# Kernel optimization log

Hardware: AMD Instinct MI355X
Metric: run time of the kernel (lower is better)

Reference implementation:

```python
import jax, jax.numpy as jnp
import numpy as np

B, H, W, D, K = 64, 32, 32, 512, 64
EPS = 1e-12


def setup_inputs() -> dict:
    key = jax.random.key(0)
    k1, k2, k3 = jax.random.split(key, 3)
    inputs = jax.random.normal(k1, (B, H, W, D), dtype=jnp.float32)
    # 1x1 conv kernel (no bias) -> equivalent to a [D, K] matmul per pixel
    w = jax.random.normal(k2, (D, K), dtype=jnp.float32) * 0.02
    # cluster centers, stored in the original as (1,1,1,D,K); we keep [D, K]
    C = jax.random.normal(k3, (D, K), dtype=jnp.float32) * 0.02
    return {"inputs": inputs, "w": w, "C": C}


def _l2norm(v, axis=-1):
    return v / jnp.sqrt(jnp.sum(v * v, axis=axis, keepdims=True) + EPS)


def reference(inputs, w, C):
    # soft-assignment: 1x1 conv + softmax over clusters
    s = jnp.einsum('bhwd,dk->bhwk', inputs, w)          # [B,H,W,K]
    a = jax.nn.softmax(s, axis=-1)
    b, h, ww, d = inputs.shape
    k = w.shape[1]
    a2 = a.reshape(b, h * ww, k)                         # [B,N,K]
    x2 = inputs.reshape(b, h * ww, d)                    # [B,N,D]
    # VLAD reformulation: sum_n a[n,k]*(x[n,d] + C[d,k])
    #  = (a^T x)[k,d] + (sum_n a[n,k]) * C[d,k]
    # avoids materializing the [B,H,W,D,K] broadcast of the original
    vkd = jnp.einsum('bnk,bnd->bkd', a2, x2)             # [B,K,D]
    vkd = vkd + a2.sum(axis=1)[:, :, None] * C.T[None]   # [B,K,D]
    # intra-normalization over D (matches transpose->normalize in original)
    vkd = _l2norm(vkd, axis=-1)
    # transpose back to [B,D,K], flatten, global L2 normalize
    v = jnp.transpose(vkd, (0, 2, 1)).reshape(b, d * k)
    v = _l2norm(v, axis=-1)
    return v
```

## Files before the change

### kernel.cpp

```cpp
#include <hip/hip_runtime.h>

#define EPS 1e-12f
typedef __attribute__((ext_vector_type(8))) short short8;
typedef __attribute__((ext_vector_type(4))) float f32x4;

#define MFMA(a, b, c) __builtin_amdgcn_mfma_f32_16x16x32_bf16(a, b, c, 0, 0, 0)

__device__ __forceinline__ unsigned rne16(unsigned u) {
  return u + 0x7FFFu + ((u >> 16) & 1u);
}
__device__ __forceinline__ void split2(float f, unsigned short& h,
                                       unsigned short& l) {
  unsigned u = __float_as_uint(f);
  unsigned rh = rne16(u);
  float hf = __uint_as_float(rh & 0xFFFF0000u);
  unsigned rl = rne16(__float_as_uint(f - hf));
  h = (unsigned short)(rh >> 16);
  l = (unsigned short)(rl >> 16);
}
__device__ __forceinline__ void split_pair(float f0, float f1,
                                           unsigned& hp, unsigned& lp) {
  unsigned u0 = __float_as_uint(f0), u1 = __float_as_uint(f1);
  unsigned r0 = rne16(u0), r1 = rne16(u1);
  float h0 = __uint_as_float(r0 & 0xFFFF0000u);
  float h1 = __uint_as_float(r1 & 0xFFFF0000u);
  hp = (r0 >> 16) | (r1 & 0xFFFF0000u);
  unsigned v0 = rne16(__float_as_uint(f0 - h0));
  unsigned v1 = rne16(__float_as_uint(f1 - h1));
  lp = (v0 >> 16) | (v1 & 0xFFFF0000u);
}
__device__ __forceinline__ void split8(float4 a, float4 b, short8& h, short8& l) {
  union { unsigned u[4]; short8 s; } H, L;
  split_pair(a.x, a.y, H.u[0], L.u[0]);
  split_pair(a.z, a.w, H.u[1], L.u[1]);
  split_pair(b.x, b.y, H.u[2], L.u[2]);
  split_pair(b.z, b.w, H.u[3], L.u[3]);
  h = H.s; l = L.s;
}

extern "C" __global__ __launch_bounds__(256) void netvlad_prep(
    const float* __restrict__ w, unsigned short* __restrict__ wTh,
    unsigned short* __restrict__ wTl)
{
  int tg = blockIdx.x * 256 + threadIdx.x;
  int k = tg >> 9, d = tg & 511;
  unsigned short h, l;
  split2(w[d * 64 + k], h, l);
  wTh[tg] = h;
  wTl[tg] = l;
}

extern "C" __global__ __launch_bounds__(256) void netvlad_assign(
    const float* __restrict__ x, const unsigned short* __restrict__ wTh,
    const unsigned short* __restrict__ wTl, unsigned short* __restrict__ aTh,
    unsigned short* __restrict__ aTl, float* __restrict__ asum)
{
  __shared__ unsigned short ath[64 * 72];
  __shared__ unsigned short atl[64 * 72];
  __shared__ float asp[4 * 64];

  const int t = threadIdx.x;
  const int lane = t & 63, wv = t >> 6;
  const int lo4 = lane & 15, hi4 = lane >> 4;
  const int b = blockIdx.x >> 4;
  const int nblk = (blockIdx.x & 15) << 6;

  f32x4 acc[4] = {};

  const float* xp =
      x + ((size_t)(blockIdx.x << 6) + (wv << 4) + lo4) * 512 + (hi4 << 3);

  float4 c0 = *(const float4*)xp;
  float4 c1 = *(const float4*)(xp + 4);
  for (int d0 = 0; d0 < 512; d0 += 32) {
    const float* np = xp + ((d0 < 480) ? d0 + 32 : 0);
    float4 n0v = *(const float4*)np;
    float4 n1v = *(const float4*)(np + 4);
    short8 xh, xl;
    split8(c0, c1, xh, xl);
#pragma unroll
    for (int nt = 0; nt < 4; ++nt) {
      const size_t wo = (size_t)((nt << 4) + lo4) * 512 + d0 + (hi4 << 3);
      short8 wh = *(const short8*)(wTh + wo);
      short8 wl = *(const short8*)(wTl + wo);
      acc[nt] = MFMA(xh, wh, acc[nt]);
      acc[nt] = MFMA(xl, wh, acc[nt]);
      acc[nt] = MFMA(xh, wl, acc[nt]);
    }
    c0 = n0v; c1 = n1v;
  }

  float asum_p[4] = {0.f, 0.f, 0.f, 0.f};
#pragma unroll
  for (int r = 0; r < 4; ++r) {
    float s0 = acc[0][r], s1 = acc[1][r], s2 = acc[2][r], s3 = acc[3][r];
    float m = fmaxf(fmaxf(s0, s1), fmaxf(s2, s3));
    m = fmaxf(m, __shfl_xor(m, 1));
    m = fmaxf(m, __shfl_xor(m, 2));
    m = fmaxf(m, __shfl_xor(m, 4));
    m = fmaxf(m, __shfl_xor(m, 8));
    float e0 = __expf(s0 - m), e1 = __expf(s1 - m);
    float e2 = __expf(s2 - m), e3 = __expf(s3 - m);
    float s = e0 + e1 + e2 + e3;
    s += __shfl_xor(s, 1);
    s += __shfl_xor(s, 2);
    s += __shfl_xor(s, 4);
    s += __shfl_xor(s, 8);
    float inv = 1.0f / s;
    e0 *= inv; e1 *= inv; e2 *= inv; e3 *= inv;
    asum_p[0] += e0; asum_p[1] += e1; asum_p[2] += e2; asum_p[3] += e3;
    acc[0][r] = e0; acc[1][r] = e1; acc[2][r] = e2; acc[3][r] = e3;
  }
#pragma unroll
  for (int nt = 0; nt < 4; ++nt)
#pragma unroll
    for (int r = 0; r < 4; ++r) {
      unsigned short h, l;
      split2(acc[nt][r], h, l);
      int idx = ((nt << 4) + lo4) * 72 + (wv << 4) + (hi4 << 2) + r;
      ath[idx] = h;
      atl[idx] = l;
    }
#pragma unroll
  for (int nt = 0; nt < 4; ++nt) {
    float v = asum_p[nt];
    v += __shfl_xor(v, 16);
    v += __shfl_xor(v, 32);
    if (lane < 16) asp[(wv << 6) + (nt << 4) + lane] = v;
  }
  __syncthreads();
  if (t < 64) {
    float s = asp[t] + asp[64 + t] + asp[128 + t] + asp[192 + t];
    atomicAdd(&asum[(b << 6) + t], s);
  }
  {
    const int k = t >> 2, px0 = (t & 3) << 4;
    const size_t go = ((size_t)((b << 6) + k) << 10) + nblk + px0;
    *(short8*)(aTh + go)     = *(short8*)&ath[k * 72 + px0];
    *(short8*)(aTh + go + 8) = *(short8*)&ath[k * 72 + px0 + 8];
    *(short8*)(aTl + go)     = *(short8*)&atl[k * 72 + px0];
    *(short8*)(aTl + go + 8) = *(short8*)&atl[k * 72 + px0 + 8];
  }
}

extern "C" __global__ __launch_bounds__(256) void netvlad_vlad(
    const float* __restrict__ x, const unsigned short* __restrict__ aTh,
    const unsigned short* __restrict__ aTl, float* __restrict__ vkd)
{
  __shared__ unsigned short xth[2][32 * 72];
  __shared__ unsigned short xtl[2][32 * 72];
  const int t = threadIdx.x;
  const int lane = t & 63, wv = t >> 6;
  const int lo4 = lane & 15, hi4 = lane >> 4;
  const int b = blockIdx.x >> 4;
  const int ds = (blockIdx.x & 15) << 5;
  const int tn = t & 63;
  const int tdc = (t >> 6) << 3;
  const float* xsb = x + ((size_t)(b << 10)) * 512 + ds + tdc;

  f32x4 acc[2] = {};

  float4 r0 = *(const float4*)(xsb + (size_t)tn * 512);
  float4 r1 = *(const float4*)(xsb + (size_t)tn * 512 + 4);

  for (int it = 0; it < 16; ++it) {
    const int n0 = it << 6;
    unsigned short* th = xth[it & 1];
    unsigned short* tl = xtl[it & 1];
    float f[8] = {r0.x, r0.y, r0.z, r0.w, r1.x, r1.y, r1.z, r1.w};
#pragma unroll
    for (int j = 0; j < 8; ++j) {
      unsigned short h, l;
      split2(f[j], h, l);
      th[(tdc + j) * 72 + tn] = h;
      tl[(tdc + j) * 72 + tn] = l;
    }
    __syncthreads();
    if (it < 15) {
      const float* p = xsb + (size_t)(n0 + 64 + tn) * 512;
      r0 = *(const float4*)p;
      r1 = *(const float4*)(p + 4);
    }
#pragma unroll
    for (int nf = 0; nf < 2; ++nf) {
      const size_t ao = ((size_t)((b << 6) + (wv << 4) + lo4) << 10)
                      + n0 + (nf << 5) + (hi4 << 3);
      short8 ah = *(const short8*)(aTh + ao);
      short8 al = *(const short8*)(aTl + ao);
#pragma unroll
      for (int dt = 0; dt < 2; ++dt) {
        const int xo = ((dt << 4) + lo4) * 72 + (nf << 5) + (hi4 << 3);
        short8 bh = *(short8*)&th[xo];
        short8 bl = *(short8*)&tl[xo];
        acc[dt] = MFMA(ah, bh, acc[dt]);
        acc[dt] = MFMA(ah, bl, acc[dt]);
        acc[dt] = MFMA(al, bh, acc[dt]);
      }
    }
  }
#pragma unroll
  for (int dt = 0; dt < 2; ++dt) {
    float* vb = vkd + (((size_t)(b << 9) + ds + (dt << 4) + lo4) << 6)
              + (wv << 4) + (hi4 << 2);
    *(float4*)vb = make_float4(acc[dt][0], acc[dt][1], acc[dt][2], acc[dt][3]);
  }
}

extern "C" __global__ __launch_bounds__(256) void netvlad_fin1(
    const float* __restrict__ vkd, const float* __restrict__ Cm,
    const float* __restrict__ asum, float* __restrict__ out,
    float* __restrict__ r_buf)
{
  __shared__ float rp[16 * 64];
  const int t = threadIdx.x;
  const int b = blockIdx.x >> 4;
  const int ds = (blockIdx.x & 15) << 5;
  const int k4 = (t & 15) << 2;
  const int dg = t >> 4;
  float4 asv = *(const float4*)(asum + (b << 6) + k4);
  float4 racc = {0.f, 0.f, 0.f, 0.f};
#pragma unroll
  for (int j = 0; j < 2; ++j) {
    int d = ds + dg * 2 + j;
    size_t off = (((size_t)(b << 9) + d) << 6) + k4;
    float4 v = *(const float4*)(vkd + off);
    float4 c = *(const float4*)(Cm + ((size_t)d << 6) + k4);
    v.x += asv.x * c.x; v.y += asv.y * c.y;
    v.z += asv.z * c.z; v.w += asv.w * c.w;
    *(float4*)(out + off) = v;
    racc.x = fmaf(v.x, v.x, racc.x); racc.y = fmaf(v.y, v.y, racc.y);
    racc.z = fmaf(v.z, v.z, racc.z); racc.w = fmaf(v.w, v.w, racc.w);
  }
  *(float4*)&rp[dg * 64 + k4] = racc;
  __syncthreads();
  if (t < 64) {
    float r = 0.f;
#pragma unroll
    for (int g = 0; g < 16; ++g) r += rp[g * 64 + t];
    atomicAdd(&r_buf[(b << 6) + t], r);
  }
}

extern "C" __global__ __launch_bounds__(256) void netvlad_fin3(
    float* __restrict__ out, const float* __restrict__ r_buf)
{
  __shared__ float sc[64];
  const int t = threadIdx.x;
  const int b = blockIdx.x >> 3;
  if (t < 64) {
    float r = r_buf[(b << 6) + t];
    float g = r / (r + EPS);
    g += __shfl_xor(g, 1);
    g += __shfl_xor(g, 2);
    g += __shfl_xor(g, 4);
    g += __shfl_xor(g, 8);
    g += __shfl_xor(g, 16);
    g += __shfl_xor(g, 32);
    sc[t] = 1.0f / (sqrtf(r + EPS) * sqrtf(g + EPS));
  }
  __syncthreads();
  float4* o4 = (float4*)out;
#pragma unroll
  for (int c = 0; c < 4; ++c) {
    int idx = blockIdx.x * 1024 + c * 256 + t;
    float4 v = o4[idx];
    int k4 = (idx & 15) * 4;
    v.x *= sc[k4]; v.y *= sc[k4 + 1]; v.z *= sc[k4 + 2]; v.w *= sc[k4 + 3];
    o4[idx] = v;
  }
}

extern "C" void kernel_launch(void* const* d_in, const int* in_sizes, int n_in,
                              void* d_out, int out_size, void* d_ws,
                              size_t ws_size, hipStream_t stream)
{
  const float* x  = (const float*)d_in[0];
  const float* w  = (const float*)d_in[1];
  const float* Cm = (const float*)d_in[2];
  float* out = (float*)d_out;

  unsigned short* aTh = (unsigned short*)d_ws;
  unsigned short* aTl = aTh + 4194304;
  float* vkd = (float*)(aTl + 4194304);
  unsigned short* wTh = (unsigned short*)(vkd + 2097152);
  unsigned short* wTl = wTh + 32768;
  float* asum = (float*)(wTl + 32768);
  float* r_buf = asum + 4096;

  hipMemsetAsync(asum, 0, 2 * 4096 * sizeof(float), stream);

  netvlad_prep  <<< 128, 256, 0, stream>>>(w, wTh, wTl);
  netvlad_assign<<<1024, 256, 0, stream>>>(x, wTh, wTl, aTh, aTl, asum);
  netvlad_vlad  <<<1024, 256, 0, stream>>>(x, aTh, aTl, vkd);
  netvlad_fin1  <<<1024, 256, 0, stream>>>(vkd, Cm, asum, out, r_buf);
  netvlad_fin3  <<< 512, 256, 0, stream>>>(out, r_buf);
}
```

Baseline: 294.6 us.

## Double-buffer weight and assignment fragments in registers across assign and vlad loops

In the assign kernel, the w-fragment loads for the next 32-wide d step are now prefetched into double-buffered registers alongside the x prefetch, and the loop is fully unrolled. In the vlad kernel, the assignment fragments are prefetched one iteration ahead, and the x tile staging into LDS is reorganised so each thread writes packed pixel pairs into rows padded to 74 shorts. Both kernels get a 4-blocks-per-CU occupancy hint. The aim is to hide global-load latency behind the MFMA work. The cost is higher register pressure, and 128-bit LDS reads at a 148-byte row stride are no longer 16-byte aligned.

```diff
diff --git a/kernel.cpp b/kernel.cpp
--- a/kernel.cpp
+++ b/kernel.cpp
@@ -50,7 +50,7 @@
   wTl[tg] = l;
 }
 
-extern "C" __global__ __launch_bounds__(256) void netvlad_assign(
+extern "C" __global__ __launch_bounds__(256, 4) void netvlad_assign(
     const float* __restrict__ x, const unsigned short* __restrict__ wTh,
     const unsigned short* __restrict__ wTl, unsigned short* __restrict__ aTh,
     unsigned short* __restrict__ aTl, float* __restrict__ asum)
@@ -69,25 +69,39 @@
 
   const float* xp =
       x + ((size_t)(blockIdx.x << 6) + (wv << 4) + lo4) * 512 + (hi4 << 3);
-
-  float4 c0 = *(const float4*)xp;
-  float4 c1 = *(const float4*)(xp + 4);
-  for (int d0 = 0; d0 < 512; d0 += 32) {
-    const float* np = xp + ((d0 < 480) ? d0 + 32 : 0);
-    float4 n0v = *(const float4*)np;
-    float4 n1v = *(const float4*)(np + 4);
+  const unsigned short* wph = wTh + (lo4 << 9) + (hi4 << 3);
+  const unsigned short* wpl = wTl + (lo4 << 9) + (hi4 << 3);
+
+  float4 xc0[2], xc1[2];
+  short8 wh[2][4], wl[2][4];
+
+  xc0[0] = *(const float4*)xp;
+  xc1[0] = *(const float4*)(xp + 4);
+#pragma unroll
+  for (int nt = 0; nt < 4; ++nt) {
+    wh[0][nt] = *(const short8*)(wph + nt * 8192);
+    wl[0][nt] = *(const short8*)(wpl + nt * 8192);
+  }
+
+#pragma unroll
+  for (int it = 0; it < 16; ++it) {
+    const int cur = it & 1, nxt = cur ^ 1;
+    const int dn = ((it + 1) & 15) << 5;
+    xc0[nxt] = *(const float4*)(xp + dn);
+    xc1[nxt] = *(const float4*)(xp + dn + 4);
+#pragma unroll
+    for (int nt = 0; nt < 4; ++nt) {
+      wh[nxt][nt] = *(const short8*)(wph + nt * 8192 + dn);
+      wl[nxt][nt] = *(const short8*)(wpl + nt * 8192 + dn);
+    }
     short8 xh, xl;
-    split8(c0, c1, xh, xl);
+    split8(xc0[cur], xc1[cur], xh, xl);
 #pragma unroll
     for (int nt = 0; nt < 4; ++nt) {
-      const size_t wo = (size_t)((nt << 4) + lo4) * 512 + d0 + (hi4 << 3);
-      short8 wh = *(const short8*)(wTh + wo);
-      short8 wl = *(const short8*)(wTl + wo);
-      acc[nt] = MFMA(xh, wh, acc[nt]);
-      acc[nt] = MFMA(xl, wh, acc[nt]);
-      acc[nt] = MFMA(xh, wl, acc[nt]);
-    }
-    c0 = n0v; c1 = n1v;
+      acc[nt] = MFMA(xh, wh[cur][nt], acc[nt]);
+      acc[nt] = MFMA(xl, wh[cur][nt], acc[nt]);
+      acc[nt] = MFMA(xh, wl[cur][nt], acc[nt]);
+    }
   }
 
   float asum_p[4] = {0.f, 0.f, 0.f, 0.f};
@@ -143,60 +157,81 @@
   }
 }
 
-extern "C" __global__ __launch_bounds__(256) void netvlad_vlad(
+extern "C" __global__ __launch_bounds__(256, 4) void netvlad_vlad(
     const float* __restrict__ x, const unsigned short* __restrict__ aTh,
     const unsigned short* __restrict__ aTl, float* __restrict__ vkd)
 {
-  __shared__ unsigned short xth[2][32 * 72];
-  __shared__ unsigned short xtl[2][32 * 72];
+  __shared__ unsigned short xth[2][32 * 74];
+  __shared__ unsigned short xtl[2][32 * 74];
   const int t = threadIdx.x;
   const int lane = t & 63, wv = t >> 6;
   const int lo4 = lane & 15, hi4 = lane >> 4;
   const int b = blockIdx.x >> 4;
   const int ds = (blockIdx.x & 15) << 5;
-  const int tn = t & 63;
-  const int tdc = (t >> 6) << 3;
-  const float* xsb = x + ((size_t)(b << 10)) * 512 + ds + tdc;
+  const int np2 = (t & 31) << 1;
+  const int dc = (t >> 5) << 2;
+  const float* xsb = x + ((size_t)(b << 10)) * 512 + ds + dc;
+  const unsigned short* aph =
+      aTh + ((size_t)((b << 6) + (wv << 4) + lo4) << 10) + (hi4 << 3);
+  const unsigned short* apl =
+      aTl + ((size_t)((b << 6) + (wv << 4) + lo4) << 10) + (hi4 << 3);
 
   f32x4 acc[2] = {};
-
-  float4 r0 = *(const float4*)(xsb + (size_t)tn * 512);
-  float4 r1 = *(const float4*)(xsb + (size_t)tn * 512 + 4);
-
+  float4 xr0, xr1;
+  short8 ah[2][2], al[2][2];
+
+  xr0 = *(const float4*)(xsb + (size_t)np2 * 512);
+  xr1 = *(const float4*)(xsb + (size_t)(np2 + 1) * 512);
+#pragma unroll
+  for (int nf = 0; nf < 2; ++nf) {
+    ah[0][nf] = *(const short8*)(aph + (nf << 5));
+    al[0][nf] = *(const short8*)(apl + (nf << 5));
+  }
+
+#pragma unroll
   for (int it = 0; it < 16; ++it) {
+    const int cur = it & 1, nxt = cur ^ 1;
     const int n0 = it << 6;
-    unsigned short* th = xth[it & 1];
-    unsigned short* tl = xtl[it & 1];
-    float f[8] = {r0.x, r0.y, r0.z, r0.w, r1.x, r1.y, r1.z, r1.w};
-#pragma unroll
-    for (int j = 0; j < 8; ++j) {
-      unsigned short h, l;
-      split2(f[j], h, l);
-      th[(tdc + j) * 72 + tn] = h;
-      tl[(tdc + j) * 72 + tn] = l;
+    unsigned short* th = xth[cur];
+    unsigned short* tl = xtl[cur];
+    {
+      float f0[4] = {xr0.x, xr0.y, xr0.z, xr0.w};
+      float f1[4] = {xr1.x, xr1.y, xr1.z, xr1.w};
+#pragma unroll
+      for (int j = 0; j < 4; ++j) {
+        unsigned short h0, l0, h1, l1;
+        split2(f0[j], h0, l0);
+        split2(f1[j], h1, l1);
+        ushort2 hp; hp.x = h0; hp.y = h1;
+        ushort2 lp; lp.x = l0; lp.y = l1;
+        *(ushort2*)&th[(dc + j) * 74 + np2] = hp;
+        *(ushort2*)&tl[(dc + j) * 74 + np2] = lp;
+      }
     }
     __syncthreads();
     if (it < 15) {
-      const float* p = xsb + (size_t)(n0 + 64 + tn) * 512;
-      r0 = *(const float4*)p;
-      r1 = *(const float4*)(p + 4);
-    }
-#pragma unroll
-    for (int nf = 0; nf < 2; ++nf) {
-      const size_t ao = ((size_t)((b << 6) + (wv << 4) + lo4) << 10)
-                      + n0 + (nf << 5) + (hi4 << 3);
-      short8 ah = *(const short8*)(aTh + ao);
-      short8 al = *(const short8*)(aTl + ao);
+      xr0 = *(const float4*)(xsb + (size_t)(n0 + 64 + np2) * 512);
+      xr1 = *(const float4*)(xsb + (size_t)(n0 + 64 + np2 + 1) * 512);
+    }
+    {
+      const int nn = ((it + 1) & 15) << 6;
+#pragma unroll
+      for (int nf = 0; nf < 2; ++nf) {
+        ah[nxt][nf] = *(const short8*)(aph + nn + (nf << 5));
+        al[nxt][nf] = *(const short8*)(apl + nn + (nf << 5));
+      }
+    }
+#pragma unroll
+    for (int nf = 0; nf < 2; ++nf)
 #pragma unroll
       for (int dt = 0; dt < 2; ++dt) {
-        const int xo = ((dt << 4) + lo4) * 72 + (nf << 5) + (hi4 << 3);
+        const int xo = ((dt << 4) + lo4) * 74 + (nf << 5) + (hi4 << 3);
         short8 bh = *(short8*)&th[xo];
         short8 bl = *(short8*)&tl[xo];
-        acc[dt] = MFMA(ah, bh, acc[dt]);
-        acc[dt] = MFMA(ah, bl, acc[dt]);
-        acc[dt] = MFMA(al, bh, acc[dt]);
+        acc[dt] = MFMA(ah[cur][nf], bh, acc[dt]);
+        acc[dt] = MFMA(ah[cur][nf], bl, acc[dt]);
+        acc[dt] = MFMA(al[cur][nf], bh, acc[dt]);
       }
-    }
   }
 #pragma unroll
   for (int dt = 0; dt < 2; ++dt) {
```

Measured after the change: 310.2 us. 5.3% more time.
